# Kernel tuning notes

Measured on AMD Instinct MI355X. Metric: run time of the kernel, lower is better.

The kernel has to match this reference:

```python
import jax, jax.numpy as jnp
from jax import lax
import numpy as np

B, N, NP, NS = 32, 4096, 512, 16
C = 256            # seed_feat_dim
RADIUS = 0.3
EPS = 1e-5         # BatchNorm eps
HID = 128


def setup_inputs() -> dict:
    key = jax.random.key(0)
    ks = jax.random.split(key, 8)
    xyz = jax.random.normal(ks[0], (B, N, 3), jnp.float32)
    features = jax.random.normal(ks[1], (B, C, N), jnp.float32)
    seed_xyz = jax.random.normal(ks[2], (B, N, 3), jnp.float32)
    c_in = C + 3  # use_xyz=True -> mlp[0] += 3
    def conv_w(k, cin, cout):
        return jax.random.normal(k, (cout, cin), jnp.float32) * (1.0 / np.sqrt(cin))
    w1 = conv_w(ks[3], c_in, HID)
    w2 = conv_w(ks[4], HID, HID)
    w3 = conv_w(ks[5], HID, HID)
    ones = jnp.ones((HID,), jnp.float32)
    zeros = jnp.zeros((HID,), jnp.float32)
    return dict(xyz=xyz, features=features, seed_xyz=seed_xyz,
                w1=w1, g1=ones, be1=zeros,
                w2=w2, g2=ones, be2=zeros,
                w3=w3, g3=ones, be3=zeros)


def furthest_point_sample(pts, npoint):
    # pts: (B, N, 3) -> (B, npoint) int32
    Bb, Nn, _ = pts.shape
    first = jnp.zeros((Bb,), jnp.int32)
    dists0 = jnp.full((Bb, Nn), 1e10, pts.dtype)
    def step(carry, _):
        dists, last = carry
        lp = jnp.take_along_axis(pts, last[:, None, None], axis=1)  # (B,1,3)
        d = jnp.sum((pts - lp) ** 2, axis=-1)                        # (B,N)
        dists = jnp.minimum(dists, d)
        nxt = jnp.argmax(dists, axis=-1).astype(jnp.int32)
        return (dists, nxt), nxt
    _, rest = lax.scan(step, (dists0, first), None, length=npoint - 1)
    return jnp.concatenate([first[None, :], rest], axis=0).T  # (B, npoint)


def ball_query(new_xyz, xyz, radius, nsample):
    # new_xyz: (B,NP,3), xyz: (B,N,3) -> (B,NP,nsample) int32
    d2 = jnp.sum((new_xyz[:, :, None, :] - xyz[:, None, :, :]) ** 2, axis=-1)  # (B,NP,N)
    Nn = xyz.shape[1]
    # first `nsample` indices (in index order) inside radius, like the CUDA kernel
    score = jnp.where(d2 < radius * radius, jnp.arange(Nn, dtype=jnp.int32)[None, None, :], Nn)
    neg_vals, _ = lax.top_k(-score, nsample)   # largest of -score = smallest indices
    idx = -neg_vals                            # (B,NP,nsample)
    valid = idx < Nn
    idx = jnp.where(valid, idx, idx[:, :, 0:1])  # pad with first hit (query point itself)
    return idx


def _conv_bn_relu(x, w, g, be):
    # x: (B,Cin,NP,NS); 1x1 Conv2d (no bias, bn=True) + BatchNorm2d (training stats) + ReLU
    y = jnp.einsum('oc,bcps->bops', w, x)
    m = y.mean(axis=(0, 2, 3))
    v = y.var(axis=(0, 2, 3))
    y = (y - m[None, :, None, None]) * (g / jnp.sqrt(v + EPS))[None, :, None, None] + be[None, :, None, None]
    return jax.nn.relu(y)


def reference(xyz, features, seed_xyz, w1, g1, be1, w2, g2, be2, w3, g3, be3):
    # sampling == 'seed_fps'
    sample_inds = furthest_point_sample(seed_xyz, NP)                 # (B,NP)
    new_xyz = jnp.take_along_axis(xyz, sample_inds[:, :, None], axis=1)  # (B,NP,3)
    idx = ball_query(new_xyz, xyz, RADIUS, NS)                        # (B,NP,NS)
    grouped_xyz = jax.vmap(lambda p, i: p[i])(xyz, idx)               # (B,NP,NS,3)
    grouped_xyz = (grouped_xyz - new_xyz[:, :, None, :]) / RADIUS     # normalize_xyz=True
    grouped_feat = jax.vmap(lambda f, i: f[:, i])(features, idx)      # (B,C,NP,NS)
    x = jnp.concatenate([grouped_xyz.transpose(0, 3, 1, 2), grouped_feat], axis=1)  # (B,3+C,NP,NS)
    x = _conv_bn_relu(x, w1, g1, be1)
    x = _conv_bn_relu(x, w2, g2, be2)
    x = _conv_bn_relu(x, w3, g3, be3)
    new_features = jnp.max(x, axis=-1)                                # (B,128,NP)
    return new_xyz, new_features, sample_inds
```

## Files before the change

### kernel.cpp

```cpp
#include <hip/hip_runtime.h>
#include <cstdint>
#include <cstddef>

#define B   32
#define N   4096
#define NP  512
#define NS  16
#define C   256
#define CIN 259
#define HID 128
#define SB  (NP*NS)
#define S   (B*SB)
#define EPSF 1e-5f

#define FPS_BLOCKS 32
#define TR_BLOCKS  (B*256)
#define PREP_BLOCKS 64

#define NREP 32
#define LSTRIDE (NREP*256)

typedef __attribute__((ext_vector_type(8))) short short8;
typedef __attribute__((ext_vector_type(4))) float floatx4;

__device__ __forceinline__ float bf2f(unsigned short u) {
    return __uint_as_float(((unsigned)u) << 16);
}
__device__ __forceinline__ unsigned short f2bf(float f) {
    unsigned u = __float_as_uint(f);
    return (unsigned short)((u + 0x7FFFu + ((u >> 16) & 1u)) >> 16);
}

__device__ __forceinline__ int wave_max_i32(int x) {
    int y;
    y = __builtin_amdgcn_update_dpp(0, x, 0x111, 0xf, 0xf, true); x = (y > x) ? y : x;
    y = __builtin_amdgcn_update_dpp(0, x, 0x112, 0xf, 0xf, true); x = (y > x) ? y : x;
    y = __builtin_amdgcn_update_dpp(0, x, 0x114, 0xf, 0xf, true); x = (y > x) ? y : x;
    y = __builtin_amdgcn_update_dpp(0, x, 0x118, 0xf, 0xf, true); x = (y > x) ? y : x;
    y = __builtin_amdgcn_update_dpp(0, x, 0x142, 0xa, 0xf, true); x = (y > x) ? y : x;
    y = __builtin_amdgcn_update_dpp(0, x, 0x143, 0xc, 0xf, true); x = (y > x) ? y : x;
    return __builtin_amdgcn_readlane(x, 63);
}
__device__ __forceinline__ unsigned wave_max_u32(unsigned x) {
    unsigned y;
    y = (unsigned)__builtin_amdgcn_update_dpp(0, (int)x, 0x111, 0xf, 0xf, true); x = (y > x) ? y : x;
    y = (unsigned)__builtin_amdgcn_update_dpp(0, (int)x, 0x112, 0xf, 0xf, true); x = (y > x) ? y : x;
    y = (unsigned)__builtin_amdgcn_update_dpp(0, (int)x, 0x114, 0xf, 0xf, true); x = (y > x) ? y : x;
    y = (unsigned)__builtin_amdgcn_update_dpp(0, (int)x, 0x118, 0xf, 0xf, true); x = (y > x) ? y : x;
    y = (unsigned)__builtin_amdgcn_update_dpp(0, (int)x, 0x142, 0xa, 0xf, true); x = (y > x) ? y : x;
    y = (unsigned)__builtin_amdgcn_update_dpp(0, (int)x, 0x143, 0xc, 0xf, true); x = (y > x) ? y : x;
    return (unsigned)__builtin_amdgcn_readlane((int)x, 63);
}

__device__ __forceinline__ unsigned long long umax64(unsigned long long a, unsigned long long b) {
    return (b > a) ? b : a;
}

__device__ __forceinline__ float row16_sum(float x) {
    float y;
    y = __int_as_float(__builtin_amdgcn_update_dpp(0, __float_as_int(x), 0x111, 0xf, 0xf, true)); x += y;
    y = __int_as_float(__builtin_amdgcn_update_dpp(0, __float_as_int(x), 0x112, 0xf, 0xf, true)); x += y;
    y = __int_as_float(__builtin_amdgcn_update_dpp(0, __float_as_int(x), 0x114, 0xf, 0xf, true)); x += y;
    y = __int_as_float(__builtin_amdgcn_update_dpp(0, __float_as_int(x), 0x118, 0xf, 0xf, true)); x += y;
    return x;
}
__device__ __forceinline__ float row16_max(float x) {
    int xi = __float_as_int(x);
    float y;
    y = __int_as_float(__builtin_amdgcn_update_dpp(xi, xi, 0x111, 0xf, 0xf, false)); x = fmaxf(x, y); xi = __float_as_int(x);
    y = __int_as_float(__builtin_amdgcn_update_dpp(xi, xi, 0x112, 0xf, 0xf, false)); x = fmaxf(x, y); xi = __float_as_int(x);
    y = __int_as_float(__builtin_amdgcn_update_dpp(xi, xi, 0x114, 0xf, 0xf, false)); x = fmaxf(x, y); xi = __float_as_int(x);
    y = __int_as_float(__builtin_amdgcn_update_dpp(xi, xi, 0x118, 0xf, 0xf, false)); x = fmaxf(x, y);
    return x;
}

__global__ __launch_bounds__(512) void fused_front_kernel(
        const float* __restrict__ seed, const float* __restrict__ xyz,
        const float* __restrict__ feat, const float* __restrict__ w1,
        const float* __restrict__ w2, const float* __restrict__ w3,
        unsigned short* __restrict__ featT, unsigned short* __restrict__ w1fb,
        unsigned short* __restrict__ w2b, unsigned short* __restrict__ w3b,
        float* __restrict__ stats, int* __restrict__ inds,
        float* __restrict__ out_newxyz, float* __restrict__ out_inds_f) {
    __shared__ float smem[3 * N];
    __shared__ __align__(16) unsigned long long skey[2][8];
    __shared__ __align__(16) float4 scoord[2][8];
    __shared__ int lhist[NP];
    int bid = blockIdx.x;
    int t = threadIdx.x;

    if (bid >= FPS_BLOCKS) {
        int hb = bid - FPS_BLOCKS;
        if (hb < TR_BLOCKS) {
            float* ls = smem;
            int b2 = hb >> 8, rem = hb & 255;
            int ct = rem >> 5, jt = rem & 31;
            int c0 = ct * 32, j0 = jt * 128;
            const float* src = feat + (size_t)b2 * C * N;
            #pragma unroll
            for (int i = 0; i < 8; i++) {
                int lin = t + 512 * i;
                int jj = lin & 127, cc = lin >> 7;
                ls[cc * 129 + jj] = src[(size_t)(c0 + cc) * N + j0 + jj];
            }
            __syncthreads();
            int c8 = t & 3, jj = t >> 2;
            unsigned pk[4];
            #pragma unroll
            for (int q = 0; q < 4; q++) {
                float f0 = ls[(c8 * 8 + 2 * q) * 129 + jj];
                float f1 = ls[(c8 * 8 + 2 * q + 1) * 129 + jj];
                pk[q] = (unsigned)f2bf(f0) | ((unsigned)f2bf(f1) << 16);
            }
            *(uint4*)&featT[((size_t)b2 * N + j0 + jj) * 256 + c0 + c8 * 8] =
                make_uint4(pk[0], pk[1], pk[2], pk[3]);
        } else {
            int i0 = (hb - TR_BLOCKS) * 512 + t;
            if (i0 < 256 * HID) { int o = i0 >> 8, k = i0 & 255; w1fb[i0] = f2bf(w1[o * CIN + 3 + k]); }
            if (i0 < HID * HID) { w2b[i0] = f2bf(w2[i0]); w3b[i0] = f2bf(w3[i0]); }
            if (i0 < 3 * LSTRIDE) stats[i0] = 0.f;
        }
        return;
    }

    int b = bid;
    const float* sp = seed + (size_t)b * N * 3;
    float px[8], py[8], pz[8], dloc[8];
    #pragma unroll
    for (int u = 0; u < 8; u++) {
        int i = t + 512 * u;
        px[u] = sp[i * 3 + 0]; py[u] = sp[i * 3 + 1]; pz[u] = sp[i * 3 + 2];
        dloc[u] = 1e10f;
    }
    if (t == 0) lhist[0] = 0;
    float lx = sp[0], ly = sp[1], lz = sp[2];
    int lane = t & 63, w = t >> 6;
    for (int k = 1; k < NP; k++) {
        float bv = -1.f; int bi = 0;
        float bx = 0.f, by = 0.f, bz = 0.f;
        #pragma unroll
        for (int u = 0; u < 8; u++) {
            int i = t + 512 * u;
            float dx = __fsub_rn(px[u], lx);
            float dy = __fsub_rn(py[u], ly);
            float dz = __fsub_rn(pz[u], lz);
            float d  = __fadd_rn(__fadd_rn(__fmul_rn(dx, dx), __fmul_rn(dy, dy)), __fmul_rn(dz, dz));
            float dm = fminf(dloc[u], d);
            dloc[u] = dm;
            bool bt = dm > bv;
            bv = bt ? dm : bv;
            bi = bt ? i : bi;
            bx = bt ? px[u] : bx;
            by = bt ? py[u] : by;
            bz = bt ? pz[u] : bz;
        }
        int wm = wave_max_i32(__float_as_int(bv));
        unsigned cand = (__float_as_int(bv) == wm) ? ~(unsigned)bi : 0u;
        unsigned winv = wave_max_u32(cand);
        int wbi = (int)(~winv);
        int par = k & 1;
        if (lane == (wbi & 63)) {
            skey[par][w] = (((unsigned long long)(unsigned)wm) << 12) | (unsigned)(4095 - wbi);
            scoord[par][w] = make_float4(bx, by, bz, 0.f);
        }
        __syncthreads();
        const ulonglong2* kp = (const ulonglong2*)&skey[par][0];
        ulonglong2 q0 = kp[0], q1 = kp[1], q2 = kp[2], q3 = kp[3];
        unsigned long long a = umax64(q0.x, q0.y);
        unsigned long long c2 = umax64(q1.x, q1.y);
        unsigned long long e = umax64(q2.x, q2.y);
        unsigned long long g = umax64(q3.x, q3.y);
        unsigned long long h = umax64(umax64(a, c2), umax64(e, g));
        int gi = 4095 - (int)(h & 0xFFFull);
        int ws = (gi & 511) >> 6;
        float4 wc = scoord[par][ws];
        lx = wc.x; ly = wc.y; lz = wc.z;
        if (t == 0) lhist[k] = gi;
    }
    __syncthreads();
    {
        int p = t;
        int j = lhist[p];
        const float* xb = xyz + ((size_t)b * N + j) * 3;
        float* ob = out_newxyz + ((size_t)b * NP + p) * 3;
        ob[0] = xb[0]; ob[1] = xb[1]; ob[2] = xb[2];
        out_inds_f[b * NP + p] = (float)j;
    }
}

__global__ __launch_bounds__(256) void ballquery_kernel(const float* __restrict__ xyz,
        const float* __restrict__ newxyz, int* __restrict__ idx) {
    __shared__ float sx[N], sy[N], sz[N];
    int blk = blockIdx.x;
    int b   = blk >> 5;
    int q00 = (blk & 31) * 16;
    int t = threadIdx.x, lane = t & 63, w = t >> 6;
    const float* xb = xyz + (size_t)b * N * 3;
    for (int i = t; i < N; i += 256) { sx[i] = xb[i * 3]; sy[i] = xb[i * 3 + 1]; sz[i] = xb[i * 3 + 2]; }
    __syncthreads();
    for (int qi = 0; qi < 4; qi++) {
        int q = q00 + w * 4 + qi;
        const float* nq = newxyz + ((size_t)(b * NP + q)) * 3;
        float qx = nq[0], qy = nq[1], qz = nq[2];
        int* out = idx + ((size_t)(b * NP + q)) * NS;
        int cnt = 0, first = -1;
        for (int it = 0; it < 64; it++) {
            int j = it * 64 + lane;
            float dx = __fsub_rn(sx[j], qx);
            float dy = __fsub_rn(sy[j], qy);
            float dz = __fsub_rn(sz[j], qz);
            float d2 = __fadd_rn(__fadd_rn(__fmul_rn(dx, dx), __fmul_rn(dy, dy)), __fmul_rn(dz, dz));
            bool inb = d2 < 0.09f;
            unsigned long long m = __ballot(inb);
            if (m) {
                if (first < 0) first = it * 64 + __builtin_ctzll(m);
                if (inb) {
                    int r = cnt + __popcll(m & ((1ull << lane) - 1ull));
                    if (r < NS) out[r] = j;
                }
                cnt += __popcll(m);
                if (cnt >= NS) break;
            }
        }
        if (cnt < NS && lane >= cnt && lane < NS) out[lane] = first;
    }
}

__global__ __launch_bounds__(256) void gemm1_mfma(
        const unsigned short* __restrict__ w1fb, const float* __restrict__ w1raw,
        const unsigned short* __restrict__ featT, const float* __restrict__ newxyz,
        const float* __restrict__ xyz, const int* __restrict__ idx,
        unsigned short* __restrict__ y1, float* __restrict__ statsOut) {
    __shared__ unsigned short Xs[128][136];
    __shared__ float xn0[128], xn1[128], xn2[128];
    __shared__ int jl[128];
    int t = threadIdx.x;
    int s0 = blockIdx.x * 128;
    int b = s0 >> 13;
    if (t < 128) {
        int pn = (s0 & (SB - 1)) + t;
        int p = pn >> 4, n = pn & 15;
        int j = idx[((size_t)(b * NP + p)) * NS + n];
        jl[t] = j;
        const float* xb = xyz + ((size_t)(b * N + j)) * 3;
        const float* nq = newxyz + ((size_t)(b * NP + p)) * 3;
        xn0[t] = (xb[0] - nq[0]) / 0.3f;
        xn1[t] = (xb[1] - nq[1]) / 0.3f;
        xn2[t] = (xb[2] - nq[2]) / 0.3f;
    }
    __syncthreads();
    int lane = t & 63, w = t >> 6;
    int row16 = lane & 15, quad = lane >> 4;
    floatx4 acc[2][8];
    #pragma unroll
    for (int mt = 0; mt < 2; mt++)
        #pragma unroll
        for (int nt = 0; nt < 8; nt++)
            acc[mt][nt] = (floatx4){0.f, 0.f, 0.f, 0.f};
    int ss = t >> 1, hh = (t & 1) * 64;
    const unsigned short* grow = featT + ((size_t)b * N + jl[ss]) * 256 + hh;
    for (int slab = 0; slab < 2; slab++) {
        int k0 = slab * 128;
        {
            const uint4* src = (const uint4*)(grow + k0);
            #pragma unroll
            for (int i = 0; i < 8; i++)
                *(uint4*)&Xs[ss][hh + i * 8] = src[i];
        }
        __syncthreads();
        #pragma unroll
        for (int kk = 0; kk < 128; kk += 32) {
            short8 a0 = *(const short8*)&w1fb[(size_t)(w * 32 + row16) * 256 + k0 + kk + quad * 8];
            short8 a1 = *(const short8*)&w1fb[(size_t)(w * 32 + 16 + row16) * 256 + k0 + kk + quad * 8];
            #pragma unroll
            for (int nt = 0; nt < 8; nt++) {
                short8 bf = *(const short8*)&Xs[nt * 16 + row16][kk + quad * 8];
                acc[0][nt] = __builtin_amdgcn_mfma_f32_16x16x32_bf16(a0, bf, acc[0][nt], 0, 0, 0);
                acc[1][nt] = __builtin_amdgcn_mfma_f32_16x16x32_bf16(a1, bf, acc[1][nt], 0, 0, 0);
            }
        }
        __syncthreads();
    }
    float wa[8], wbv[8], wc[8];
    #pragma unroll
    for (int mt = 0; mt < 2; mt++)
        #pragma unroll
        for (int r = 0; r < 4; r++) {
            int o = w * 32 + mt * 16 + quad * 4 + r;
            const float* wr = w1raw + (size_t)o * CIN;
            wa[mt * 4 + r] = wr[0]; wbv[mt * 4 + r] = wr[1]; wc[mt * 4 + r] = wr[2];
        }
    float x0l[8], x1l[8], x2l[8];
    #pragma unroll
    for (int nt = 0; nt < 8; nt++) {
        int s = nt * 16 + row16;
        x0l[nt] = xn0[s]; x1l[nt] = xn1[s]; x2l[nt] = xn2[s];
    }
    float s8[2][4] = {}, q8[2][4] = {};
    #pragma unroll
    for (int mt = 0; mt < 2; mt++)
        #pragma unroll
        for (int nt = 0; nt < 8; nt++) {
            int s = nt * 16 + row16;
            int ob = w * 32 + mt * 16 + quad * 4;
            floatx4 a = acc[mt][nt];
            float v0 = a[0] + wa[mt*4+0]*x0l[nt] + wbv[mt*4+0]*x1l[nt] + wc[mt*4+0]*x2l[nt];
            float v1 = a[1] + wa[mt*4+1]*x0l[nt] + wbv[mt*4+1]*x1l[nt] + wc[mt*4+1]*x2l[nt];
            float v2 = a[2] + wa[mt*4+2]*x0l[nt] + wbv[mt*4+2]*x1l[nt] + wc[mt*4+2]*x2l[nt];
            float v3 = a[3] + wa[mt*4+3]*x0l[nt] + wbv[mt*4+3]*x1l[nt] + wc[mt*4+3]*x2l[nt];
            s8[mt][0] += v0; q8[mt][0] = fmaf(v0, v0, q8[mt][0]);
            s8[mt][1] += v1; q8[mt][1] = fmaf(v1, v1, q8[mt][1]);
            s8[mt][2] += v2; q8[mt][2] = fmaf(v2, v2, q8[mt][2]);
            s8[mt][3] += v3; q8[mt][3] = fmaf(v3, v3, q8[mt][3]);
            unsigned p0 = (unsigned)f2bf(v0) | ((unsigned)f2bf(v1) << 16);
            unsigned p1 = (unsigned)f2bf(v2) | ((unsigned)f2bf(v3) << 16);
            *(uint2*)&Xs[s][ob] = make_uint2(p0, p1);
        }
    {
        int rep = (blockIdx.x & (NREP - 1)) * 256;
        #pragma unroll
        for (int mt = 0; mt < 2; mt++)
            #pragma unroll
            for (int r = 0; r < 4; r++) {
                float sv = row16_sum(s8[mt][r]);
                float qv = row16_sum(q8[mt][r]);
                if ((lane & 15) == 15) {
                    int o = w * 32 + mt * 16 + quad * 4 + r;
                    atomicAdd(&statsOut[rep + o], sv);
                    atomicAdd(&statsOut[rep + 128 + o], qv);
                }
            }
    }
    __syncthreads();
    int c = t & 15, sr = t >> 4;
    #pragma unroll
    for (int i = 0; i < 8; i++) {
        int s = sr + 16 * i;
        uint4 v = *(const uint4*)&Xs[s][c * 8];
        *(uint4*)&y1[(size_t)(s0 + s) * 128 + c * 8] = v;
    }
}

__global__ __launch_bounds__(256) void gemm_bn_mfma(
        const unsigned short* __restrict__ wb16, const unsigned short* __restrict__ yprev,
        const float* __restrict__ statsPrev, const float* __restrict__ gPrev,
        const float* __restrict__ bePrev, float* __restrict__ statsOut,
        unsigned short* __restrict__ yout) {
    __shared__ unsigned short Xs[128][136];
    __shared__ float ssc[128], ssh[128];
    int t = threadIdx.x;
    int s0 = blockIdx.x * 128;
    if (t < 128) {
        float sA = 0.f, qA = 0.f;
        #pragma unroll
        for (int r = 0; r < NREP; r++) {
            sA += statsPrev[r * 256 + t];
            qA += statsPrev[r * 256 + 128 + t];
        }
        float mean = sA * (1.f / (float)S);
        float var  = qA * (1.f / (float)S) - mean * mean;
        float sc = gPrev[t] / sqrtf(var + EPSF);
        ssc[t] = sc;
        ssh[t] = bePrev[t] - mean * sc;
    }
    __syncthreads();
    int ss = t >> 1, hh = (t & 1) * 64;
    {
        const uint4* src = (const uint4*)&yprev[(size_t)(s0 + ss) * 128 + hh];
        #pragma unroll
        for (int i = 0; i < 8; i++) {
            uint4 raw = src[i];
            int kb = hh + i * 8;
            float4 c0 = *(float4*)&ssc[kb];
            float4 c1 = *(float4*)&ssc[kb + 4];
            float4 h0 = *(float4*)&ssh[kb];
            float4 h1 = *(float4*)&ssh[kb + 4];
            float f0 = fmaxf(0.f, fmaf(bf2f((unsigned short)(raw.x & 0xFFFF)), c0.x, h0.x));
            float f1 = fmaxf(0.f, fmaf(bf2f((unsigned short)(raw.x >> 16)),    c0.y, h0.y));
            float f2 = fmaxf(0.f, fmaf(bf2f((unsigned short)(raw.y & 0xFFFF)), c0.z, h0.z));
            float f3 = fmaxf(0.f, fmaf(bf2f((unsigned short)(raw.y >> 16)),    c0.w, h0.w));
            float f4 = fmaxf(0.f, fmaf(bf2f((unsigned short)(raw.z & 0xFFFF)), c1.x, h1.x));
            float f5 = fmaxf(0.f, fmaf(bf2f((unsigned short)(raw.z >> 16)),    c1.y, h1.y));
            float f6 = fmaxf(0.f, fmaf(bf2f((unsigned short)(raw.w & 0xFFFF)), c1.z, h1.z));
            float f7 = fmaxf(0.f, fmaf(bf2f((unsigned short)(raw.w >> 16)),    c1.w, h1.w));
            unsigned o0 = (unsigned)f2bf(f0) | ((unsigned)f2bf(f1) << 16);
            unsigned o1 = (unsigned)f2bf(f2) | ((unsigned)f2bf(f3) << 16);
            unsigned o2 = (unsigned)f2bf(f4) | ((unsigned)f2bf(f5) << 16);
            unsigned o3 = (unsigned)f2bf(f6) | ((unsigned)f2bf(f7) << 16);
            *(uint4*)&Xs[ss][kb] = make_uint4(o0, o1, o2, o3);
        }
    }
    __syncthreads();
    int lane = t & 63, w = t >> 6;
    int row16 = lane & 15, quad = lane >> 4;
    floatx4 acc[2][8];
    #pragma unroll
    for (int mt = 0; mt < 2; mt++)
        #pragma unroll
        for (int nt = 0; nt < 8; nt++)
            acc[mt][nt] = (floatx4){0.f, 0.f, 0.f, 0.f};
    #pragma unroll
    for (int kk = 0; kk < 128; kk += 32) {
        short8 a0 = *(const short8*)&wb16[(size_t)(w * 32 + row16) * 128 + kk + quad * 8];
        short8 a1 = *(const short8*)&wb16[(size_t)(w * 32 + 16 + row16) * 128 + kk + quad * 8];
        #pragma unroll
        for (int nt = 0; nt < 8; nt++) {
            short8 bf = *(const short8*)&Xs[nt * 16 + row16][kk + quad * 8];
            acc[0][nt] = __builtin_amdgcn_mfma_f32_16x16x32_bf16(a0, bf, acc[0][nt], 0, 0, 0);
            acc[1][nt] = __builtin_amdgcn_mfma_f32_16x16x32_bf16(a1, bf, acc[1][nt], 0, 0, 0);
        }
    }
    __syncthreads();
    float s8[2][4] = {}, q8[2][4] = {};
    #pragma unroll
    for (int mt = 0; mt < 2; mt++)
        #pragma unroll
        for (int nt = 0; nt < 8; nt++) {
            int s = nt * 16 + row16;
            int ob = w * 32 + mt * 16 + quad * 4;
            floatx4 a = acc[mt][nt];
            s8[mt][0] += a[0]; q8[mt][0] = fmaf(a[0], a[0], q8[mt][0]);
            s8[mt][1] += a[1]; q8[mt][1] = fmaf(a[1], a[1], q8[mt][1]);
            s8[mt][2] += a[2]; q8[mt][2] = fmaf(a[2], a[2], q8[mt][2]);
            s8[mt][3] += a[3]; q8[mt][3] = fmaf(a[3], a[3], q8[mt][3]);
            unsigned p0 = (unsigned)f2bf(a[0]) | ((unsigned)f2bf(a[1]) << 16);
            unsigned p1 = (unsigned)f2bf(a[2]) | ((unsigned)f2bf(a[3]) << 16);
            *(uint2*)&Xs[s][ob] = make_uint2(p0, p1);
        }
    {
        int rep = (blockIdx.x & (NREP - 1)) * 256;
        #pragma unroll
        for (int mt = 0; mt < 2; mt++)
            #pragma unroll
            for (int r = 0; r < 4; r++) {
                float sv = row16_sum(s8[mt][r]);
                float qv = row16_sum(q8[mt][r]);
                if ((lane & 15) == 15) {
                    int o = w * 32 + mt * 16 + quad * 4 + r;
                    atomicAdd(&statsOut[rep + o], sv);
                    atomicAdd(&statsOut[rep + 128 + o], qv);
                }
            }
    }
    __syncthreads();
    int c = t & 15, sr = t >> 4;
    #pragma unroll
    for (int i = 0; i < 8; i++) {
        int s = sr + 16 * i;
        uint4 v = *(const uint4*)&Xs[s][c * 8];
        *(uint4*)&yout[(size_t)(s0 + s) * 128 + c * 8] = v;
    }
}

__global__ __launch_bounds__(256) void gemm3_pool_mfma(
        const unsigned short* __restrict__ wb16, const unsigned short* __restrict__ yprev,
        const float* __restrict__ statsPrev, const float* __restrict__ gPrev,
        const float* __restrict__ bePrev, float* __restrict__ statsOut,
        float* __restrict__ out_feat) {
    __shared__ unsigned short Xs[128][136];
    __shared__ float ssc[128], ssh[128];
    __shared__ float pool[8][133];
    int t = threadIdx.x;
    int s0 = blockIdx.x * 128;
    if (t < 128) {
        float sA = 0.f, qA = 0.f;
        #pragma unroll
        for (int r = 0; r < NREP; r++) {
            sA += statsPrev[r * 256 + t];
            qA += statsPrev[r * 256 + 128 + t];
        }
        float mean = sA * (1.f / (float)S);
        float var  = qA * (1.f / (float)S) - mean * mean;
        float sc = gPrev[t] / sqrtf(var + EPSF);
        ssc[t] = sc;
        ssh[t] = bePrev[t] - mean * sc;
    }
    __syncthreads();
    int ss = t >> 1, hh = (t & 1) * 64;
    {
        const uint4* src = (const uint4*)&yprev[(size_t)(s0 + ss) * 128 + hh];
        #pragma unroll
        for (int i = 0; i < 8; i++) {
            uint4 raw = src[i];
            int kb = hh + i * 8;
            float4 c0 = *(float4*)&ssc[kb];
            float4 c1 = *(float4*)&ssc[kb + 4];
            float4 h0 = *(float4*)&ssh[kb];
            float4 h1 = *(float4*)&ssh[kb + 4];
            float f0 = fmaxf(0.f, fmaf(bf2f((unsigned short)(raw.x & 0xFFFF)), c0.x, h0.x));
            float f1 = fmaxf(0.f, fmaf(bf2f((unsigned short)(raw.x >> 16)),    c0.y, h0.y));
            float f2 = fmaxf(0.f, fmaf(bf2f((unsigned short)(raw.y & 0xFFFF)), c0.z, h0.z));
            float f3 = fmaxf(0.f, fmaf(bf2f((unsigned short)(raw.y >> 16)),    c0.w, h0.w));
            float f4 = fmaxf(0.f, fmaf(bf2f((unsigned short)(raw.z & 0xFFFF)), c1.x, h1.x));
            float f5 = fmaxf(0.f, fmaf(bf2f((unsigned short)(raw.z >> 16)),    c1.y, h1.y));
            float f6 = fmaxf(0.f, fmaf(bf2f((unsigned short)(raw.w & 0xFFFF)), c1.z, h1.z));
            float f7 = fmaxf(0.f, fmaf(bf2f((unsigned short)(raw.w >> 16)),    c1.w, h1.w));
            unsigned o0 = (unsigned)f2bf(f0) | ((unsigned)f2bf(f1) << 16);
            unsigned o1 = (unsigned)f2bf(f2) | ((unsigned)f2bf(f3) << 16);
            unsigned o2 = (unsigned)f2bf(f4) | ((unsigned)f2bf(f5) << 16);
            unsigned o3 = (unsigned)f2bf(f6) | ((unsigned)f2bf(f7) << 16);
            *(uint4*)&Xs[ss][kb] = make_uint4(o0, o1, o2, o3);
        }
    }
    __syncthreads();
    int lane = t & 63, w = t >> 6;
    int row16 = lane & 15, quad = lane >> 4;
    floatx4 acc[2][8];
    #pragma unroll
    for (int mt = 0; mt < 2; mt++)
        #pragma unroll
        for (int nt = 0; nt < 8; nt++)
            acc[mt][nt] = (floatx4){0.f, 0.f, 0.f, 0.f};
    #pragma unroll
    for (int kk = 0; kk < 128; kk += 32) {
        short8 a0 = *(const short8*)&wb16[(size_t)(w * 32 + row16) * 128 + kk + quad * 8];
        short8 a1 = *(const short8*)&wb16[(size_t)(w * 32 + 16 + row16) * 128 + kk + quad * 8];
        #pragma unroll
        for (int nt = 0; nt < 8; nt++) {
            short8 bf = *(const short8*)&Xs[nt * 16 + row16][kk + quad * 8];
            acc[0][nt] = __builtin_amdgcn_mfma_f32_16x16x32_bf16(a0, bf, acc[0][nt], 0, 0, 0);
            acc[1][nt] = __builtin_amdgcn_mfma_f32_16x16x32_bf16(a1, bf, acc[1][nt], 0, 0, 0);
        }
    }
    float s8[2][4] = {}, q8[2][4] = {};
    #pragma unroll
    for (int mt = 0; mt < 2; mt++)
        #pragma unroll
        for (int nt = 0; nt < 8; nt++) {
            floatx4 a = acc[mt][nt];
            #pragma unroll
            for (int r = 0; r < 4; r++) {
                float v = a[r];
                s8[mt][r] += v;
                q8[mt][r] = fmaf(v, v, q8[mt][r]);
                float mx = row16_max(v);
                if ((lane & 15) == 15)
                    pool[nt][w * 32 + mt * 16 + quad * 4 + r] = mx;
            }
        }
    {
        int rep = (blockIdx.x & (NREP - 1)) * 256;
        #pragma unroll
        for (int mt = 0; mt < 2; mt++)
            #pragma unroll
            for (int r = 0; r < 4; r++) {
                float sv = row16_sum(s8[mt][r]);
                float qv = row16_sum(q8[mt][r]);
                if ((lane & 15) == 15) {
                    int o = w * 32 + mt * 16 + quad * 4 + r;
                    atomicAdd(&statsOut[rep + o], sv);
                    atomicAdd(&statsOut[rep + 128 + o], qv);
                }
            }
    }
    __syncthreads();
    {
        int b = s0 >> 13;
        int pcol0 = (s0 & (SB - 1)) >> 4;
        int o = t >> 1, half = (t & 1) * 4;
        float4 v = make_float4(pool[half + 0][o], pool[half + 1][o],
                               pool[half + 2][o], pool[half + 3][o]);
        *(float4*)&out_feat[((size_t)b * HID + o) * NP + pcol0 + half] = v;
    }
}

__global__ __launch_bounds__(256) void finalize_kernel(float* __restrict__ out_feat,
        const float* __restrict__ st3, const float* __restrict__ g,
        const float* __restrict__ be) {
    __shared__ float lsc[8], lsh[8];
    int blk = blockIdx.x;
    int t = threadIdx.x;
    int base = blk * 4096;
    int o0 = (blk * 8) & 127;
    if (t < 8) {
        int o = o0 + t;
        float sA = 0.f, qA = 0.f;
        #pragma unroll
        for (int r = 0; r < NREP; r++) {
            sA += st3[r * 256 + o];
            qA += st3[r * 256 + 128 + o];
        }
        float mean = sA * (1.f / (float)S);
        float var  = qA * (1.f / (float)S) - mean * mean;
        float sc = g[o] / sqrtf(var + EPSF);
        lsc[t] = sc;
        lsh[t] = be[o] - mean * sc;
    }
    __syncthreads();
    int i = base + t * 16;
    int oloc = (t * 16) >> 9;
    float sc = lsc[oloc], sh = lsh[oloc];
    float4* p = (float4*)&out_feat[i];
    #pragma unroll
    for (int j = 0; j < 4; j++) {
        float4 v = p[j];
        v.x = fmaxf(0.f, fmaf(v.x, sc, sh));
        v.y = fmaxf(0.f, fmaf(v.y, sc, sh));
        v.z = fmaxf(0.f, fmaf(v.z, sc, sh));
        v.w = fmaxf(0.f, fmaf(v.w, sc, sh));
        p[j] = v;
    }
}

extern "C" void kernel_launch(void* const* d_in, const int* in_sizes, int n_in,
                              void* d_out, int out_size, void* d_ws, size_t ws_size,
                              hipStream_t stream) {
    const float* xyz  = (const float*)d_in[0];
    const float* feat = (const float*)d_in[1];
    const float* seed = (const float*)d_in[2];
    const float* w1 = (const float*)d_in[3];
    const float* g1 = (const float*)d_in[4];
    const float* be1 = (const float*)d_in[5];
    const float* w2 = (const float*)d_in[6];
    const float* g2 = (const float*)d_in[7];
    const float* be2 = (const float*)d_in[8];
    const float* w3 = (const float*)d_in[9];
    const float* g3 = (const float*)d_in[10];
    const float* be3 = (const float*)d_in[11];

    float* out_newxyz = (float*)d_out;
    float* out_feat   = out_newxyz + B * NP * 3;
    float* out_inds   = out_feat + B * HID * NP;

    float* stats = (float*)d_ws;
    int*   inds  = (int*)(stats + 3 * LSTRIDE);
    int*   idx   = inds + B * NP;
    unsigned short* w1fb  = (unsigned short*)(idx + (size_t)B * NP * NS);
    unsigned short* w2b   = w1fb + 256 * HID;
    unsigned short* w3b   = w2b + HID * HID;
    unsigned short* featT = w3b + HID * HID;
    unsigned short* y1    = featT + (size_t)B * N * 256;
    unsigned short* y2    = featT;

    size_t need = (size_t)(3 * LSTRIDE) * 4 + (size_t)B * NP * 4 + (size_t)B * NP * NS * 4
                + (size_t)(256 * HID + 2 * HID * HID) * 2
                + 2ull * (size_t)B * N * 256 * 2;
    if (ws_size < need) return;

    fused_front_kernel<<<FPS_BLOCKS + TR_BLOCKS + PREP_BLOCKS, 512, 0, stream>>>(
        seed, xyz, feat, w1, w2, w3, featT, w1fb, w2b, w3b, stats,
        inds, out_newxyz, out_inds);
    ballquery_kernel<<<B * 32, 256, 0, stream>>>(xyz, out_newxyz, idx);
    gemm1_mfma<<<S / 128, 256, 0, stream>>>(w1fb, w1, featT, out_newxyz, xyz, idx, y1, stats);
    gemm_bn_mfma<<<S / 128, 256, 0, stream>>>(w2b, y1, stats, g1, be1, stats + LSTRIDE, y2);
    gemm3_pool_mfma<<<S / 128, 256, 0, stream>>>(w3b, y2, stats + LSTRIDE, g2, be2, stats + 2 * LSTRIDE, out_feat);
    finalize_kernel<<<(B * HID * NP) / 4096, 256, 0, stream>>>(out_feat, stats + 2 * LSTRIDE, g3, be3);
}
```

Baseline: 740.0 us.

## Use single 64-bit wave max in FPS and swizzle gemm1 block order

The FPS loop packs each thread's best distance and index into one 64-bit key and does a single DPP wave max, where it used to run two 32-bit reductions. The winning point's coordinates are now read from shared-memory copies of the seed points rather than carried through the reduction. This shortens the serial per-iteration critical path of the 511-step FPS loop, at the cost of staging the points in LDS and doing twice the DPP moves per reduction step. Separately, gemm1 remaps blockIdx through an XCD-style interleave (pb&7)*256+(pb>>3), so that blocks on the same XCD work on contiguous sample ranges for better L2 locality.

Measured after the change: 711.4 us. -3.9%, faster.

```diff
diff --git a/kernel.cpp b/kernel.cpp
--- a/kernel.cpp
+++ b/kernel.cpp
@@ -31,25 +31,21 @@
     return (unsigned short)((u + 0x7FFFu + ((u >> 16) & 1u)) >> 16);
 }
 
-__device__ __forceinline__ int wave_max_i32(int x) {
-    int y;
-    y = __builtin_amdgcn_update_dpp(0, x, 0x111, 0xf, 0xf, true); x = (y > x) ? y : x;
-    y = __builtin_amdgcn_update_dpp(0, x, 0x112, 0xf, 0xf, true); x = (y > x) ? y : x;
-    y = __builtin_amdgcn_update_dpp(0, x, 0x114, 0xf, 0xf, true); x = (y > x) ? y : x;
-    y = __builtin_amdgcn_update_dpp(0, x, 0x118, 0xf, 0xf, true); x = (y > x) ? y : x;
-    y = __builtin_amdgcn_update_dpp(0, x, 0x142, 0xa, 0xf, true); x = (y > x) ? y : x;
-    y = __builtin_amdgcn_update_dpp(0, x, 0x143, 0xc, 0xf, true); x = (y > x) ? y : x;
-    return __builtin_amdgcn_readlane(x, 63);
-}
-__device__ __forceinline__ unsigned wave_max_u32(unsigned x) {
-    unsigned y;
-    y = (unsigned)__builtin_amdgcn_update_dpp(0, (int)x, 0x111, 0xf, 0xf, true); x = (y > x) ? y : x;
-    y = (unsigned)__builtin_amdgcn_update_dpp(0, (int)x, 0x112, 0xf, 0xf, true); x = (y > x) ? y : x;
-    y = (unsigned)__builtin_amdgcn_update_dpp(0, (int)x, 0x114, 0xf, 0xf, true); x = (y > x) ? y : x;
-    y = (unsigned)__builtin_amdgcn_update_dpp(0, (int)x, 0x118, 0xf, 0xf, true); x = (y > x) ? y : x;
-    y = (unsigned)__builtin_amdgcn_update_dpp(0, (int)x, 0x142, 0xa, 0xf, true); x = (y > x) ? y : x;
-    y = (unsigned)__builtin_amdgcn_update_dpp(0, (int)x, 0x143, 0xc, 0xf, true); x = (y > x) ? y : x;
-    return (unsigned)__builtin_amdgcn_readlane((int)x, 63);
+__device__ __forceinline__ unsigned long long wave_max_u64(unsigned long long x) {
+#define WM64_STEP(ctrl, rmask) { \
+        unsigned lo_ = (unsigned)x, hi_ = (unsigned)(x >> 32); \
+        unsigned ylo_ = (unsigned)__builtin_amdgcn_update_dpp(0, (int)lo_, ctrl, rmask, 0xf, true); \
+        unsigned yhi_ = (unsigned)__builtin_amdgcn_update_dpp(0, (int)hi_, ctrl, rmask, 0xf, true); \
+        unsigned long long y_ = ((unsigned long long)yhi_ << 32) | ylo_; \
+        x = (y_ > x) ? y_ : x; }
+    WM64_STEP(0x111, 0xf)
+    WM64_STEP(0x112, 0xf)
+    WM64_STEP(0x114, 0xf)
+    WM64_STEP(0x118, 0xf)
+    WM64_STEP(0x142, 0xa)
+    WM64_STEP(0x143, 0xc)
+#undef WM64_STEP
+    return x;
 }
 
 __device__ __forceinline__ unsigned long long umax64(unsigned long long a, unsigned long long b) {
@@ -84,7 +80,6 @@
         float* __restrict__ out_newxyz, float* __restrict__ out_inds_f) {
     __shared__ float smem[3 * N];
     __shared__ __align__(16) unsigned long long skey[2][8];
-    __shared__ __align__(16) float4 scoord[2][8];
     __shared__ int lhist[NP];
     int bid = blockIdx.x;
     int t = threadIdx.x;
@@ -125,19 +120,24 @@
 
     int b = bid;
     const float* sp = seed + (size_t)b * N * 3;
+    float* sx = smem;
+    float* sy = smem + N;
+    float* sz = smem + 2 * N;
     float px[8], py[8], pz[8], dloc[8];
     #pragma unroll
     for (int u = 0; u < 8; u++) {
         int i = t + 512 * u;
-        px[u] = sp[i * 3 + 0]; py[u] = sp[i * 3 + 1]; pz[u] = sp[i * 3 + 2];
+        float x = sp[i * 3 + 0], y = sp[i * 3 + 1], z = sp[i * 3 + 2];
+        sx[i] = x; sy[i] = y; sz[i] = z;
+        px[u] = x; py[u] = y; pz[u] = z;
         dloc[u] = 1e10f;
     }
     if (t == 0) lhist[0] = 0;
     float lx = sp[0], ly = sp[1], lz = sp[2];
     int lane = t & 63, w = t >> 6;
+    __syncthreads();
     for (int k = 1; k < NP; k++) {
         float bv = -1.f; int bi = 0;
-        float bx = 0.f, by = 0.f, bz = 0.f;
         #pragma unroll
         for (int u = 0; u < 8; u++) {
             int i = t + 512 * u;
@@ -150,19 +150,12 @@
             bool bt = dm > bv;
             bv = bt ? dm : bv;
             bi = bt ? i : bi;
-            bx = bt ? px[u] : bx;
-            by = bt ? py[u] : by;
-            bz = bt ? pz[u] : bz;
-        }
-        int wm = wave_max_i32(__float_as_int(bv));
-        unsigned cand = (__float_as_int(bv) == wm) ? ~(unsigned)bi : 0u;
-        unsigned winv = wave_max_u32(cand);
-        int wbi = (int)(~winv);
+        }
+        unsigned long long key =
+            (((unsigned long long)(unsigned)__float_as_int(bv)) << 12) | (unsigned)(4095 - bi);
+        unsigned long long wmax = wave_max_u64(key);
         int par = k & 1;
-        if (lane == (wbi & 63)) {
-            skey[par][w] = (((unsigned long long)(unsigned)wm) << 12) | (unsigned)(4095 - wbi);
-            scoord[par][w] = make_float4(bx, by, bz, 0.f);
-        }
+        if (lane == 63) skey[par][w] = wmax;
         __syncthreads();
         const ulonglong2* kp = (const ulonglong2*)&skey[par][0];
         ulonglong2 q0 = kp[0], q1 = kp[1], q2 = kp[2], q3 = kp[3];
@@ -172,9 +165,7 @@
         unsigned long long g = umax64(q3.x, q3.y);
         unsigned long long h = umax64(umax64(a, c2), umax64(e, g));
         int gi = 4095 - (int)(h & 0xFFFull);
-        int ws = (gi & 511) >> 6;
-        float4 wc = scoord[par][ws];
-        lx = wc.x; ly = wc.y; lz = wc.z;
+        lx = sx[gi]; ly = sy[gi]; lz = sz[gi];
         if (t == 0) lhist[k] = gi;
     }
     __syncthreads();
@@ -235,7 +226,9 @@
     __shared__ float xn0[128], xn1[128], xn2[128];
     __shared__ int jl[128];
     int t = threadIdx.x;
-    int s0 = blockIdx.x * 128;
+    int pb = blockIdx.x;
+    int lsb = (pb & 7) * 256 + (pb >> 3);
+    int s0 = lsb * 128;
     int b = s0 >> 13;
     if (t < 128) {
         int pn = (s0 & (SB - 1)) + t;
@@ -317,7 +310,7 @@
             *(uint2*)&Xs[s][ob] = make_uint2(p0, p1);
         }
     {
-        int rep = (blockIdx.x & (NREP - 1)) * 256;
+        int rep = (pb & (NREP - 1)) * 256;
         #pragma unroll
         for (int mt = 0; mt < 2; mt++)
             #pragma unroll
```
